# Kernel optimization log

Measured on AMD Instinct MI355X. Metric: run time of the kernel, lower is better.

## Reference

```python
import jax, jax.numpy as jnp
import numpy as np

EPS = 1e-15
LRELU_ALPHA = 0.2  # = init alpha


def setup_inputs() -> dict:
    key = jax.random.key(0)
    k1, k2, k3, k4 = jax.random.split(key, 4)
    N, E, F_in, F_out = 100000, 3200000, 256, 64
    inputs = jax.random.normal(k1, (N, F_in), dtype=jnp.float32)
    edge_index = jax.random.randint(k2, (2, E), 0, N, dtype=jnp.int64)
    # xavier_normal with gain 1.414
    W = jax.random.normal(k3, (F_in, F_out), dtype=jnp.float32) * (1.414 * np.sqrt(2.0 / (F_in + F_out)))
    a = jax.random.normal(k4, (1, 2 * F_out), dtype=jnp.float32) * (1.414 * np.sqrt(2.0 / (1 + 2 * F_out)))
    return {"inputs": inputs, "edge_index": edge_index, "W": W, "a": a}


def reference(inputs, edge_index, W, a):
    N = inputs.shape[0]
    F_out = W.shape[1]
    src = edge_index[0]  # row i (destination of aggregation)
    dst = edge_index[1]  # col j (neighbor being aggregated)

    h = inputs @ W  # [N, F_out]
    # values = a @ concat(h[src], h[dst]).T  ==  (h @ a1)[src] + (h @ a2)[dst]
    a1 = a[0, :F_out]
    a2 = a[0, F_out:]
    s1 = h @ a1  # [N]
    s2 = h @ a2  # [N]
    values = s1[src] + s2[dst]  # [E]
    ev_a = jax.nn.leaky_relu(values, LRELU_ALPHA)
    edge_value = jnp.exp(ev_a - jnp.max(ev_a))  # global max, as in torch code

    # e_rowsum = A @ ones  -> per-row sum of edge values
    e_rowsum = jax.ops.segment_sum(edge_value, src, num_segments=N)  # [N]
    # h_prime = A @ h (dropout p=0 -> identity)
    h_prime = jax.ops.segment_sum(edge_value[:, None] * h[dst], src, num_segments=N)  # [N, F_out]
    h_prime = h_prime / (e_rowsum[:, None] + EPS)
    return jax.nn.elu(h_prime)  # concat=True
```

## Files before the change

### kernel.cpp

```cpp
#include <hip/hip_runtime.h>
#include <hip/hip_bf16.h>
#include <math.h>

#define F_IN 256
#define F_OUT 64
#define LRELU_ALPHA 0.2f
#define EPS 1e-15f
#define CHUNK 4096
#define BSH 7
#define BNODES 128
#define NBMAX 1024
#define LCAP 4800
#define CPAD 16
#define HN 64
#define HCAP 2600

typedef __bf16 bf16x8 __attribute__((ext_vector_type(8)));
typedef float  f32x4  __attribute__((ext_vector_type(4)));

__device__ __forceinline__ unsigned int fkey(float x) {
    unsigned int u = __float_as_uint(x);
    return (u & 0x80000000u) ? ~u : (u | 0x80000000u);
}
__device__ __forceinline__ float funkey(unsigned int k) {
    return (k & 0x80000000u) ? __uint_as_float(k ^ 0x80000000u)
                             : __uint_as_float(~k);
}
__device__ __forceinline__ unsigned short f2bf(float x) {
    __hip_bfloat16 b = __float2bfloat16(x);
    return *reinterpret_cast<unsigned short*>(&b);
}
__device__ __forceinline__ float bf2f(unsigned int u) {
    return __uint_as_float(u << 16);
}

__global__ __launch_bounds__(256) void wprep(
    const float* __restrict__ W, unsigned short* __restrict__ Wt)
{
    const int i = blockIdx.x * 256 + threadIdx.x;
    const int n = i & 63;
    const int k = i >> 6;
    Wt[n * 256 + k] = f2bf(W[k * 64 + n]);
}

#define KAP 72
__global__ __launch_bounds__(256) void gemm_part(
    const float* __restrict__ X, const unsigned short* __restrict__ Wt,
    const float* __restrict__ a,
    unsigned short* __restrict__ h_bf, float* __restrict__ s1,
    float* __restrict__ s2, unsigned int* __restrict__ gsmax, int N,
    const int* __restrict__ src, const int* __restrict__ dst,
    int* __restrict__ coarse_cnt, unsigned int* __restrict__ coarse,
    int E, int NB, int GB)
{
    __shared__ __align__(16) char smem[18464];

    if (blockIdx.x < GB) {
        unsigned short* As = (unsigned short*)smem;
        float* red1 = (float*)(smem + 18432);
        float* red2 = red1 + 4;

        const int tid  = threadIdx.x;
        const int lane = tid & 63;
        const int l15  = lane & 15;
        const int quad = lane >> 4;
        const int w    = tid >> 6;
        const int n0   = blockIdx.x * 128;

        const unsigned short* wbase = Wt + l15 * 256 + quad * 8;

        f32x4 acc[2][4] = {};

        for (int c = 0; c < 4; ++c) {
            __syncthreads();
#pragma unroll
            for (int i = 0; i < 8; ++i) {
                int q   = tid + i * 256;
                int row = q >> 4;
                int k4  = q & 15;
                int gr  = n0 + row;
                float4 v = make_float4(0.f, 0.f, 0.f, 0.f);
                if (gr < N)
                    v = *(const float4*)&X[(size_t)gr * F_IN + c * 64 + k4 * 4];
                unsigned int p0 = f2bf(v.x) | ((unsigned int)f2bf(v.y) << 16);
                unsigned int p1 = f2bf(v.z) | ((unsigned int)f2bf(v.w) << 16);
                *(uint2*)&As[row * KAP + k4 * 4] = make_uint2(p0, p1);
            }
            __syncthreads();

#pragma unroll
            for (int ks = 0; ks < 64; ks += 32) {
                bf16x8 afrag[2], bfrag[4];
#pragma unroll
                for (int rt = 0; rt < 2; ++rt) {
                    uint4 ua = *(const uint4*)&As[(w * 32 + rt * 16 + l15) * KAP + ks + quad * 8];
                    afrag[rt] = __builtin_bit_cast(bf16x8, ua);
                }
#pragma unroll
                for (int ct = 0; ct < 4; ++ct) {
                    uint4 ub = *(const uint4*)&wbase[ct * 4096 + c * 64 + ks];
                    bfrag[ct] = __builtin_bit_cast(bf16x8, ub);
                }
#pragma unroll
                for (int rt = 0; rt < 2; ++rt)
#pragma unroll
                    for (int ct = 0; ct < 4; ++ct)
                        acc[rt][ct] = __builtin_amdgcn_mfma_f32_16x16x32_bf16(
                            afrag[rt], bfrag[ct], acc[rt][ct], 0, 0, 0);
            }
        }

        float a1v[4], a2v[4];
#pragma unroll
        for (int ct = 0; ct < 4; ++ct) {
            a1v[ct] = a[ct * 16 + l15];
            a2v[ct] = a[F_OUT + ct * 16 + l15];
        }
        float m1 = -INFINITY, m2 = -INFINITY;
#pragma unroll
        for (int rt = 0; rt < 2; ++rt) {
#pragma unroll
            for (int reg = 0; reg < 4; ++reg) {
                int n = n0 + w * 32 + rt * 16 + quad * 4 + reg;
                float p1 = 0.f, p2 = 0.f;
#pragma unroll
                for (int ct = 0; ct < 4; ++ct) {
                    float v = acc[rt][ct][reg];
                    p1 = fmaf(v, a1v[ct], p1);
                    p2 = fmaf(v, a2v[ct], p2);
                }
#pragma unroll
                for (int ofs = 1; ofs < 16; ofs <<= 1) {
                    p1 += __shfl_xor(p1, ofs, 64);
                    p2 += __shfl_xor(p2, ofs, 64);
                }
                if (n < N) {
#pragma unroll
                    for (int ct = 0; ct < 4; ++ct)
                        h_bf[(size_t)n * F_OUT + ct * 16 + l15] = f2bf(acc[rt][ct][reg]);
                    if (l15 == 0) { s1[n] = p1; s2[n] = p2; }
                    m1 = fmaxf(m1, p1);
                    m2 = fmaxf(m2, p2);
                }
            }
        }
#pragma unroll
        for (int ofs = 32; ofs > 0; ofs >>= 1) {
            m1 = fmaxf(m1, __shfl_xor(m1, ofs, 64));
            m2 = fmaxf(m2, __shfl_xor(m2, ofs, 64));
        }
        if (lane == 0) { red1[w] = m1; red2[w] = m2; }
        __syncthreads();
        if (tid == 0) {
            float b1 = fmaxf(fmaxf(red1[0], red1[1]), fmaxf(red1[2], red1[3]));
            float b2 = fmaxf(fmaxf(red2[0], red2[1]), fmaxf(red2[2], red2[3]));
            atomicMax(&gsmax[0], fkey(b1));
            atomicMax(&gsmax[1], fkey(b2));
        }
    } else {
        int* hist = (int*)smem;
        int* cur  = hist + NBMAX;
        const int pb = blockIdx.x - GB;
        const int e0 = pb * CHUNK;
        const int e1 = (e0 + CHUNK < E) ? e0 + CHUNK : E;
        const int nv = (e1 - e0) >> 2;
        const int4* s4p = (const int4*)(src + e0);
        const int4* d4p = (const int4*)(dst + e0);

        for (int i = threadIdx.x; i < NB; i += 256) hist[i] = 0;
        __syncthreads();

        for (int i = threadIdx.x; i < nv; i += 256) {
            int4 s4 = s4p[i];
            atomicAdd(&hist[s4.x >> BSH], 1);
            atomicAdd(&hist[s4.y >> BSH], 1);
            atomicAdd(&hist[s4.z >> BSH], 1);
            atomicAdd(&hist[s4.w >> BSH], 1);
        }
        for (int e = e0 + (nv << 2) + threadIdx.x; e < e1; e += 256)
            atomicAdd(&hist[src[e] >> BSH], 1);
        __syncthreads();

        for (int i = threadIdx.x; i < NB; i += 256) {
            int c = hist[i];
            cur[i] = c ? atomicAdd(&coarse_cnt[(size_t)i * CPAD], c) : 0;
        }
        __syncthreads();

        for (int i = threadIdx.x; i < nv; i += 256) {
            int4 s4 = s4p[i];
            int4 d4 = d4p[i];
#define PUT(S, D)                                                          \
            {                                                              \
                int b_   = (S) >> BSH;                                     \
                int pos_ = atomicAdd(&cur[b_], 1);                         \
                if (pos_ < LCAP)                                           \
                    coarse[(size_t)b_ * LCAP + pos_] =                     \
                        ((unsigned int)(D) << BSH) |                       \
                        (unsigned int)((S) & (BNODES - 1));                \
            }
            PUT(s4.x, d4.x)
            PUT(s4.y, d4.y)
            PUT(s4.z, d4.z)
            PUT(s4.w, d4.w)
        }
        for (int e = e0 + (nv << 2) + threadIdx.x; e < e1; e += 256) {
            int s = src[e], d = dst[e];
            PUT(s, d)
        }
#undef PUT
    }
}

__global__ __launch_bounds__(512) void bin_gather(
    const unsigned int* __restrict__ coarse, const int* __restrict__ coarse_cnt,
    const float* __restrict__ s1, const float* __restrict__ s2,
    const unsigned int* __restrict__ gsmax,
    const unsigned short* __restrict__ hb, float* __restrict__ out, int N)
{
    __shared__ unsigned int leds[HCAP];
    __shared__ int   hcnt[HN];
    __shared__ int   hinc[HN];
    __shared__ int   curs[HN];
    __shared__ float s1s[HN];

    const int b   = blockIdx.x >> 1;
    const int sub = blockIdx.x & 1;
    const int t   = threadIdx.x;
    const int n0  = (b << BSH) + (sub << 6);
    int cnt = coarse_cnt[(size_t)b * CPAD];
    if (cnt > LCAP) cnt = LCAP;
    const unsigned int* cb = coarse + (size_t)b * LCAP;

    if (t < HN) {
        hcnt[t] = 0;
        s1s[t] = (n0 + t < N) ? s1[n0 + t] : 0.f;
    }
    __syncthreads();

    for (int e = t; e < cnt; e += 512) {
        unsigned int p = cb[e];
        if (((p >> 6) & 1u) == (unsigned int)sub)
            atomicAdd(&hcnt[p & (HN - 1)], 1);
    }
    __syncthreads();

    if (t < HN) hinc[t] = hcnt[t];
    __syncthreads();
    for (int d = 1; d < HN; d <<= 1) {
        int x = (t < HN && t >= d) ? hinc[t - d] : 0;
        __syncthreads();
        if (t < HN) hinc[t] += x;
        __syncthreads();
    }
    if (t < HN) curs[t] = hinc[t] - hcnt[t];
    __syncthreads();

    const float M = funkey(gsmax[0]) + funkey(gsmax[1]);
    for (int e = t; e < cnt; e += 1024) {
        unsigned int p0 = cb[e];
        const int e2 = e + 512;
        const bool m0 = (((p0 >> 6) & 1u) == (unsigned int)sub);
        const bool m1b = (e2 < cnt);
        unsigned int p1 = m1b ? cb[e2] : 0u;
        const bool m1 = m1b && (((p1 >> 6) & 1u) == (unsigned int)sub);
        float sa = m0 ? s2[p0 >> BSH] : 0.f;
        float sb = m1 ? s2[p1 >> BSH] : 0.f;

        if (m0) {
            int sl = p0 & (HN - 1);
            float v = s1s[sl] + sa;
            v = fmaxf(v, LRELU_ALPHA * v);
            unsigned int wb = f2bf(__expf(v - M));
            int pos = atomicAdd(&curs[sl], 1);
            if (pos < HCAP) leds[pos] = ((p0 >> BSH) << 15) | wb;
        }
        if (m1) {
            int sl = p1 & (HN - 1);
            float v = s1s[sl] + sb;
            v = fmaxf(v, LRELU_ALPHA * v);
            unsigned int wb = f2bf(__expf(v - M));
            int pos = atomicAdd(&curs[sl], 1);
            if (pos < HCAP) leds[pos] = ((p1 >> BSH) << 15) | wb;
        }
    }
    __syncthreads();

    const int lane = t & 63;
    const int wv   = t >> 6;
    const int g    = lane >> 4;
    const int fi   = lane & 15;

    for (int i = 0; i < 8; ++i) {
        const int nl = wv * 8 + i;
        const int n  = n0 + nl;
        const bool valid = (n < N);
        int re = valid ? hinc[nl] : 0;
        int rs = valid ? re - hcnt[nl] : 0;
        if (re > HCAP) re = HCAP;
        if (rs > HCAP) rs = HCAP;

        float a0 = 0.f, a1 = 0.f, a2 = 0.f, a3 = 0.f, ws = 0.f;
        for (int bb = rs; bb < re; bb += 64) {
            const int nb = (re - bb < 64) ? re - bb : 64;
            unsigned int pv = (lane < nb) ? leds[bb + lane] : 0u;
            ws += bf2f(pv & 0x7fffu);
            for (int k = 0; k < nb; k += 16) {
                unsigned int pe0 = __shfl(pv, k + g,      64);
                unsigned int pe1 = __shfl(pv, k + 4 + g,  64);
                unsigned int pe2 = __shfl(pv, k + 8 + g,  64);
                unsigned int pe3 = __shfl(pv, k + 12 + g, 64);
                float w0 = bf2f(pe0 & 0x7fffu);
                float w1 = bf2f(pe1 & 0x7fffu);
                float w2 = bf2f(pe2 & 0x7fffu);
                float w3 = bf2f(pe3 & 0x7fffu);
                uint2 hv0 = *(const uint2*)&hb[(size_t)(pe0 >> 15) * F_OUT + fi * 4];
                uint2 hv1 = *(const uint2*)&hb[(size_t)(pe1 >> 15) * F_OUT + fi * 4];
                uint2 hv2 = *(const uint2*)&hb[(size_t)(pe2 >> 15) * F_OUT + fi * 4];
                uint2 hv3 = *(const uint2*)&hb[(size_t)(pe3 >> 15) * F_OUT + fi * 4];
                a0 = fmaf(w0, bf2f(hv0.x & 0xffffu), a0);
                a1 = fmaf(w0, bf2f(hv0.x >> 16),     a1);
                a2 = fmaf(w0, bf2f(hv0.y & 0xffffu), a2);
                a3 = fmaf(w0, bf2f(hv0.y >> 16),     a3);
                a0 = fmaf(w1, bf2f(hv1.x & 0xffffu), a0);
                a1 = fmaf(w1, bf2f(hv1.x >> 16),     a1);
                a2 = fmaf(w1, bf2f(hv1.y & 0xffffu), a2);
                a3 = fmaf(w1, bf2f(hv1.y >> 16),     a3);
                a0 = fmaf(w2, bf2f(hv2.x & 0xffffu), a0);
                a1 = fmaf(w2, bf2f(hv2.x >> 16),     a1);
                a2 = fmaf(w2, bf2f(hv2.y & 0xffffu), a2);
                a3 = fmaf(w2, bf2f(hv2.y >> 16),     a3);
                a0 = fmaf(w3, bf2f(hv3.x & 0xffffu), a0);
                a1 = fmaf(w3, bf2f(hv3.x >> 16),     a1);
                a2 = fmaf(w3, bf2f(hv3.y & 0xffffu), a2);
                a3 = fmaf(w3, bf2f(hv3.y >> 16),     a3);
            }
        }
        a0 += __shfl_xor(a0, 16, 64); a0 += __shfl_xor(a0, 32, 64);
        a1 += __shfl_xor(a1, 16, 64); a1 += __shfl_xor(a1, 32, 64);
        a2 += __shfl_xor(a2, 16, 64); a2 += __shfl_xor(a2, 32, 64);
        a3 += __shfl_xor(a3, 16, 64); a3 += __shfl_xor(a3, 32, 64);
#pragma unroll
        for (int ofs = 32; ofs > 0; ofs >>= 1)
            ws += __shfl_xor(ws, ofs, 64);

        if (valid && g == 0) {
            float inv = 1.f / (ws + EPS);
            float x0 = a0 * inv, x1 = a1 * inv, x2 = a2 * inv, x3 = a3 * inv;
            x0 = (x0 > 0.f) ? x0 : expm1f(x0);
            x1 = (x1 > 0.f) ? x1 : expm1f(x1);
            x2 = (x2 > 0.f) ? x2 : expm1f(x2);
            x3 = (x3 > 0.f) ? x3 : expm1f(x3);
            *(float4*)&out[(size_t)n * F_OUT + fi * 4] = make_float4(x0, x1, x2, x3);
        }
    }
}

extern "C" void kernel_launch(void* const* d_in, const int* in_sizes, int n_in,
                              void* d_out, int out_size, void* d_ws, size_t ws_size,
                              hipStream_t stream) {
    const float* X   = (const float*)d_in[0];
    const int*   ei  = (const int*)d_in[1];
    const float* W   = (const float*)d_in[2];
    const float* a   = (const float*)d_in[3];
    float*       out = (float*)d_out;

    const int N = in_sizes[0] / F_IN;
    const int E = in_sizes[1] / 2;
    const int* src = ei;
    const int* dst = ei + E;

    const int NB = (N + BNODES - 1) >> BSH;
    const int GB = (N + 127) / 128;
    const int PB = (E + CHUNK - 1) / CHUNK;

    unsigned short* h_bf = (unsigned short*)d_ws;
    float* s1         = (float*)(h_bf + (size_t)N * F_OUT);
    float* s2         = s1 + N;
    int*   coarse_cnt = (int*)(s2 + N);
    unsigned int* gsmax = (unsigned int*)(coarse_cnt + (size_t)NB * CPAD);
    unsigned short* Wt = (unsigned short*)(gsmax + 2);
    unsigned int* coarse = (unsigned int*)(Wt + 64 * 256);

    hipMemsetAsync(coarse_cnt, 0, ((size_t)NB * CPAD + 2) * sizeof(int), stream);

    wprep     <<<64, 256, 0, stream>>>(W, Wt);
    gemm_part <<<GB + PB, 256, 0, stream>>>(X, Wt, a, h_bf, s1, s2, gsmax, N,
                                            src, dst, coarse_cnt, coarse,
                                            E, NB, GB);
    bin_gather<<<NB * 2, 512, 0, stream>>>(coarse, coarse_cnt, s1, s2, gsmax,
                                           h_bf, out, N);
}
```

Measured before the change: 310.6 us.

## Replace global-atomic coarse bins with per-chunk local sort and offset tables

Each partition block now counting-sorts its edge chunk locally into 64-node sub-bins with a block-wide prefix scan. It writes the sorted chunk and a per-chunk offset row instead of appending to global bins through atomics. bin_gather then runs one block per 64-node sub-bin and walks every chunk's slice through the offset table, so the old two-way split that read and discarded half the edges is gone. In exchange, each gather block must read offsets from all ~780 chunks, and its threads walk short, uneven segments with scattered loads.

New measurement: 328.2 us. +5.7%, slower.

```diff
diff --git a/kernel.cpp b/kernel.cpp
--- a/kernel.cpp
+++ b/kernel.cpp
@@ -7,12 +7,9 @@
 #define LRELU_ALPHA 0.2f
 #define EPS 1e-15f
 #define CHUNK 4096
-#define BSH 7
-#define BNODES 128
-#define NBMAX 1024
-#define LCAP 4800
-#define CPAD 16
+#define BSH2 6
 #define HN 64
+#define NSBMAX 2048
 #define HCAP 2600
 
 typedef __bf16 bf16x8 __attribute__((ext_vector_type(8)));
@@ -50,8 +47,8 @@
     unsigned short* __restrict__ h_bf, float* __restrict__ s1,
     float* __restrict__ s2, unsigned int* __restrict__ gsmax, int N,
     const int* __restrict__ src, const int* __restrict__ dst,
-    int* __restrict__ coarse_cnt, unsigned int* __restrict__ coarse,
-    int E, int NB, int GB)
+    unsigned short* __restrict__ offs, unsigned int* __restrict__ coarse2,
+    int E, int NSB, int GB)
 {
     __shared__ __align__(16) char smem[18464];
 
@@ -159,52 +156,81 @@
         }
     } else {
         int* hist = (int*)smem;
-        int* cur  = hist + NBMAX;
-        const int pb = blockIdx.x - GB;
-        const int e0 = pb * CHUNK;
-        const int e1 = (e0 + CHUNK < E) ? e0 + CHUNK : E;
-        const int nv = (e1 - e0) >> 2;
+        int* cur  = hist + NSBMAX;
+        int* sums = cur + NSBMAX;
+        const int tid = threadIdx.x;
+        const int pb  = blockIdx.x - GB;
+        const int e0  = pb * CHUNK;
+        const int e1  = (e0 + CHUNK < E) ? e0 + CHUNK : E;
+        const int cntc = e1 - e0;
+        const int nv  = cntc >> 2;
         const int4* s4p = (const int4*)(src + e0);
         const int4* d4p = (const int4*)(dst + e0);
-
-        for (int i = threadIdx.x; i < NB; i += 256) hist[i] = 0;
-        __syncthreads();
-
-        for (int i = threadIdx.x; i < nv; i += 256) {
+        const int OROW = NSB + 2;
+        unsigned short* offrow = offs + (size_t)pb * OROW;
+        unsigned int*   cw     = coarse2 + (size_t)pb * CHUNK;
+
+        for (int i = tid; i < NSB; i += 256) hist[i] = 0;
+        __syncthreads();
+
+        for (int i = tid; i < nv; i += 256) {
             int4 s4 = s4p[i];
-            atomicAdd(&hist[s4.x >> BSH], 1);
-            atomicAdd(&hist[s4.y >> BSH], 1);
-            atomicAdd(&hist[s4.z >> BSH], 1);
-            atomicAdd(&hist[s4.w >> BSH], 1);
-        }
-        for (int e = e0 + (nv << 2) + threadIdx.x; e < e1; e += 256)
-            atomicAdd(&hist[src[e] >> BSH], 1);
-        __syncthreads();
-
-        for (int i = threadIdx.x; i < NB; i += 256) {
-            int c = hist[i];
-            cur[i] = c ? atomicAdd(&coarse_cnt[(size_t)i * CPAD], c) : 0;
-        }
-        __syncthreads();
-
-        for (int i = threadIdx.x; i < nv; i += 256) {
+            atomicAdd(&hist[s4.x >> BSH2], 1);
+            atomicAdd(&hist[s4.y >> BSH2], 1);
+            atomicAdd(&hist[s4.z >> BSH2], 1);
+            atomicAdd(&hist[s4.w >> BSH2], 1);
+        }
+        for (int e = e0 + (nv << 2) + tid; e < e1; e += 256)
+            atomicAdd(&hist[src[e] >> BSH2], 1);
+        __syncthreads();
+
+        const int base = tid * 8;
+        int loc[8];
+        int ssum = 0;
+#pragma unroll
+        for (int j = 0; j < 8; ++j) {
+            int idx = base + j;
+            int c = (idx < NSB) ? hist[idx] : 0;
+            loc[j] = ssum;
+            ssum += c;
+        }
+        sums[tid] = ssum;
+        __syncthreads();
+        for (int d = 1; d < 256; d <<= 1) {
+            int v = (tid >= d) ? sums[tid - d] : 0;
+            __syncthreads();
+            sums[tid] += v;
+            __syncthreads();
+        }
+        const int stripBase = sums[tid] - ssum;
+#pragma unroll
+        for (int j = 0; j < 8; ++j) {
+            int idx = base + j;
+            if (idx < NSB) {
+                int p = stripBase + loc[j];
+                cur[idx] = p;
+                offrow[idx] = (unsigned short)p;
+            }
+        }
+        if (tid == 0) offrow[NSB] = (unsigned short)cntc;
+        __syncthreads();
+
+        for (int i = tid; i < nv; i += 256) {
             int4 s4 = s4p[i];
             int4 d4 = d4p[i];
 #define PUT(S, D)                                                          \
             {                                                              \
-                int b_   = (S) >> BSH;                                     \
-                int pos_ = atomicAdd(&cur[b_], 1);                         \
-                if (pos_ < LCAP)                                           \
-                    coarse[(size_t)b_ * LCAP + pos_] =                     \
-                        ((unsigned int)(D) << BSH) |                       \
-                        (unsigned int)((S) & (BNODES - 1));                \
+                int sb_  = (S) >> BSH2;                                    \
+                int pos_ = atomicAdd(&cur[sb_], 1);                        \
+                cw[pos_] = ((unsigned int)(D) << BSH2) |                   \
+                           (unsigned int)((S) & (HN - 1));                 \
             }
             PUT(s4.x, d4.x)
             PUT(s4.y, d4.y)
             PUT(s4.z, d4.z)
             PUT(s4.w, d4.w)
         }
-        for (int e = e0 + (nv << 2) + threadIdx.x; e < e1; e += 256) {
+        for (int e = e0 + (nv << 2) + tid; e < e1; e += 256) {
             int s = src[e], d = dst[e];
             PUT(s, d)
         }
@@ -213,10 +239,11 @@
 }
 
 __global__ __launch_bounds__(512) void bin_gather(
-    const unsigned int* __restrict__ coarse, const int* __restrict__ coarse_cnt,
+    const unsigned int* __restrict__ coarse2, const unsigned short* __restrict__ offs,
     const float* __restrict__ s1, const float* __restrict__ s2,
     const unsigned int* __restrict__ gsmax,
-    const unsigned short* __restrict__ hb, float* __restrict__ out, int N)
+    const unsigned short* __restrict__ hb, float* __restrict__ out,
+    int N, int PBc, int NSB)
 {
     __shared__ unsigned int leds[HCAP];
     __shared__ int   hcnt[HN];
@@ -224,13 +251,21 @@
     __shared__ int   curs[HN];
     __shared__ float s1s[HN];
 
-    const int b   = blockIdx.x >> 1;
-    const int sub = blockIdx.x & 1;
-    const int t   = threadIdx.x;
-    const int n0  = (b << BSH) + (sub << 6);
-    int cnt = coarse_cnt[(size_t)b * CPAD];
-    if (cnt > LCAP) cnt = LCAP;
-    const unsigned int* cb = coarse + (size_t)b * LCAP;
+    const int sb = blockIdx.x;
+    const int t  = threadIdx.x;
+    const int n0 = sb << BSH2;
+    const int OROW = NSB + 2;
+
+    const int pbA = t, pbB = t + 512;
+    int oA0 = 0, oA1 = 0, oB0 = 0, oB1 = 0;
+    if (pbA < PBc) {
+        oA0 = offs[(size_t)pbA * OROW + sb];
+        oA1 = offs[(size_t)pbA * OROW + sb + 1];
+    }
+    if (pbB < PBc) {
+        oB0 = offs[(size_t)pbB * OROW + sb];
+        oB1 = offs[(size_t)pbB * OROW + sb + 1];
+    }
 
     if (t < HN) {
         hcnt[t] = 0;
@@ -238,10 +273,17 @@
     }
     __syncthreads();
 
-    for (int e = t; e < cnt; e += 512) {
-        unsigned int p = cb[e];
-        if (((p >> 6) & 1u) == (unsigned int)sub)
-            atomicAdd(&hcnt[p & (HN - 1)], 1);
+    {
+        const unsigned int* segA = coarse2 + (size_t)pbA * CHUNK;
+        for (int j = oA0; j < oA1; ++j) atomicAdd(&hcnt[segA[j] & (HN - 1)], 1);
+        const unsigned int* segB = coarse2 + (size_t)pbB * CHUNK;
+        for (int j = oB0; j < oB1; ++j) atomicAdd(&hcnt[segB[j] & (HN - 1)], 1);
+        for (int pb = t + 1024; pb < PBc; pb += 512) {
+            int o0 = offs[(size_t)pb * OROW + sb];
+            int o1 = offs[(size_t)pb * OROW + sb + 1];
+            const unsigned int* seg = coarse2 + (size_t)pb * CHUNK;
+            for (int j = o0; j < o1; ++j) atomicAdd(&hcnt[seg[j] & (HN - 1)], 1);
+        }
     }
     __syncthreads();
 
@@ -257,32 +299,29 @@
     __syncthreads();
 
     const float M = funkey(gsmax[0]) + funkey(gsmax[1]);
-    for (int e = t; e < cnt; e += 1024) {
-        unsigned int p0 = cb[e];
-        const int e2 = e + 512;
-        const bool m0 = (((p0 >> 6) & 1u) == (unsigned int)sub);
-        const bool m1b = (e2 < cnt);
-        unsigned int p1 = m1b ? cb[e2] : 0u;
-        const bool m1 = m1b && (((p1 >> 6) & 1u) == (unsigned int)sub);
-        float sa = m0 ? s2[p0 >> BSH] : 0.f;
-        float sb = m1 ? s2[p1 >> BSH] : 0.f;
-
-        if (m0) {
-            int sl = p0 & (HN - 1);
-            float v = s1s[sl] + sa;
-            v = fmaxf(v, LRELU_ALPHA * v);
-            unsigned int wb = f2bf(__expf(v - M));
-            int pos = atomicAdd(&curs[sl], 1);
-            if (pos < HCAP) leds[pos] = ((p0 >> BSH) << 15) | wb;
-        }
-        if (m1) {
-            int sl = p1 & (HN - 1);
-            float v = s1s[sl] + sb;
-            v = fmaxf(v, LRELU_ALPHA * v);
-            unsigned int wb = f2bf(__expf(v - M));
-            int pos = atomicAdd(&curs[sl], 1);
-            if (pos < HCAP) leds[pos] = ((p1 >> BSH) << 15) | wb;
-        }
+    {
+#define EMIT(P)                                                            \
+        {                                                                  \
+            unsigned int p_ = (P);                                         \
+            int sl_ = p_ & (HN - 1);                                       \
+            int d_  = p_ >> BSH2;                                          \
+            float v_ = s1s[sl_] + s2[d_];                                  \
+            v_ = fmaxf(v_, LRELU_ALPHA * v_);                              \
+            unsigned int wb_ = f2bf(__expf(v_ - M));                       \
+            int pos_ = atomicAdd(&curs[sl_], 1);                           \
+            if (pos_ < HCAP) leds[pos_] = ((unsigned int)d_ << 15) | wb_;  \
+        }
+        const unsigned int* segA = coarse2 + (size_t)pbA * CHUNK;
+        for (int j = oA0; j < oA1; ++j) EMIT(segA[j])
+        const unsigned int* segB = coarse2 + (size_t)pbB * CHUNK;
+        for (int j = oB0; j < oB1; ++j) EMIT(segB[j])
+        for (int pb = t + 1024; pb < PBc; pb += 512) {
+            int o0 = offs[(size_t)pb * OROW + sb];
+            int o1 = offs[(size_t)pb * OROW + sb + 1];
+            const unsigned int* seg = coarse2 + (size_t)pb * CHUNK;
+            for (int j = o0; j < o1; ++j) EMIT(seg[j])
+        }
+#undef EMIT
     }
     __syncthreads();
 
@@ -370,24 +409,25 @@
     const int* src = ei;
     const int* dst = ei + E;
 
-    const int NB = (N + BNODES - 1) >> BSH;
-    const int GB = (N + 127) / 128;
-    const int PB = (E + CHUNK - 1) / CHUNK;
+    const int GB  = (N + 127) / 128;
+    const int PB  = (E + CHUNK - 1) / CHUNK;
+    const int NSB = ((N + 127) / 128) * 2;
+    const int OROW = NSB + 2;
 
     unsigned short* h_bf = (unsigned short*)d_ws;
-    float* s1         = (float*)(h_bf + (size_t)N * F_OUT);
-    float* s2         = s1 + N;
-    int*   coarse_cnt = (int*)(s2 + N);
-    unsigned int* gsmax = (unsigned int*)(coarse_cnt + (size_t)NB * CPAD);
+    float* s1          = (float*)(h_bf + (size_t)N * F_OUT);
+    float* s2          = s1 + N;
+    unsigned int* gsmax = (unsigned int*)(s2 + N);
     unsigned short* Wt = (unsigned short*)(gsmax + 2);
-    unsigned int* coarse = (unsigned int*)(Wt + 64 * 256);
-
-    hipMemsetAsync(coarse_cnt, 0, ((size_t)NB * CPAD + 2) * sizeof(int), stream);
+    unsigned short* offs = Wt + 64 * 256;
+    unsigned int* coarse2 = (unsigned int*)(offs + (size_t)PB * OROW);
+
+    hipMemsetAsync(gsmax, 0, 2 * sizeof(unsigned int), stream);
 
     wprep     <<<64, 256, 0, stream>>>(W, Wt);
     gemm_part <<<GB + PB, 256, 0, stream>>>(X, Wt, a, h_bf, s1, s2, gsmax, N,
-                                            src, dst, coarse_cnt, coarse,
-                                            E, NB, GB);
-    bin_gather<<<NB * 2, 512, 0, stream>>>(coarse, coarse_cnt, s1, s2, gsmax,
-                                           h_bf, out, N);
-}
+                                            src, dst, offs, coarse2,
+                                            E, NSB, GB);
+    bin_gather<<<NSB, 512, 0, stream>>>(coarse2, offs, s1, s2, gsmax,
+                                        h_bf, out, N, PB, NSB);
+}
```
